# Optimization experiments

Measured on AMD Instinct MI355X. Metric: run time of the kernel, lower is better.

## Reference

```python
import jax, jax.numpy as jnp
import numpy as np

# GPT-2 decoder (mlm=False path of the Keras GPT module), no past/KV-cache,
# no explicit mask -> causal mask, dropout disabled (training=False).
N_HEAD = 12
NINF = -10000.0  # Attention.ninf
EPS = 1e-6


def layer_norm(x, g, b):
    m = jnp.mean(x, axis=-1, keepdims=True)
    v = jnp.mean(jnp.square(x - m), axis=-1, keepdims=True)
    return (x - m) / jnp.sqrt(v + EPS) * g + b


def gelu(x):
    # 0.5*x*(1+erf(x/sqrt(2))) as in gelu_activating
    return 0.5 * x * (1.0 + jax.lax.erf(x * np.float32(1.0 / np.sqrt(2.0))))


def setup_inputs() -> dict:
    key = jax.random.key(0)
    B, S, D, L, V, CTX = 4, 512, 768, 12, 50257, 1024
    F = 4 * D
    ks = jax.random.split(key, 10)
    init = lambda k, shape: (jax.random.normal(k, shape, jnp.float32) * 0.02)
    return {
        "x": jax.random.randint(ks[0], (B, S), 0, V),
        "emb": init(ks[1], (V, D)),        # wte (tied output projection)
        "posemb": init(ks[2], (CTX, D)),   # wpe
        "ln1_g": jnp.ones((L, D)), "ln1_b": jnp.zeros((L, D)),
        "wqkv": init(ks[3], (L, D, 3 * D)), "bqkv": jnp.zeros((L, 3 * D)),
        "wo": init(ks[4], (L, D, D)), "bo": jnp.zeros((L, D)),
        "ln2_g": jnp.ones((L, D)), "ln2_b": jnp.zeros((L, D)),
        "wfc": init(ks[5], (L, D, F)), "bfc": jnp.zeros((L, F)),
        "wproj": init(ks[6], (L, F, D)), "bproj": jnp.zeros((L, D)),
        "lnf_g": jnp.ones((D,)), "lnf_b": jnp.zeros((D,)),
    }


def reference(x, emb, posemb, ln1_g, ln1_b, wqkv, bqkv, wo, bo,
              ln2_g, ln2_b, wfc, bfc, wproj, bproj, lnf_g, lnf_b):
    B, S = x.shape
    L, D, _ = wqkv.shape
    H = N_HEAD
    hd = D // H
    scale = np.float32(1.0 / np.sqrt(hd))

    # Embedding (mlm=False): token + positional, no layernorm
    h = emb[x] + posemb[:S]  # [B,S,D]

    # causal mask: positions j > i get NINF (m1 = range(q)[:,None] < range(k)-k+q)
    mask = (jnp.arange(S)[:, None] < jnp.arange(S)[None, :]).astype(jnp.float32) * NINF

    for i in range(L):
        # pre-norm attention
        qkv = layer_norm(h, ln1_g[i], ln1_b[i]) @ wqkv[i] + bqkv[i]  # [B,S,3D]
        q, k, v = jnp.split(qkv, 3, axis=-1)
        q = q.reshape(B, S, H, hd).transpose(0, 2, 1, 3)  # [B,H,S,hd]
        k = k.reshape(B, S, H, hd).transpose(0, 2, 1, 3)
        v = v.reshape(B, S, H, hd).transpose(0, 2, 1, 3)
        scores = jnp.einsum('bhqd,bhkd->bhqk', q, k) * scale + mask
        a = jax.nn.softmax(scores, axis=-1)  # [B,H,S,S]
        o = jnp.einsum('bhqk,bhkd->bhqd', a, v)
        o = o.transpose(0, 2, 1, 3).reshape(B, S, D)
        h = h + (o @ wo[i] + bo[i])  # residual
        # pre-norm MLP
        m = layer_norm(h, ln2_g[i], ln2_b[i])
        h = h + (gelu(m @ wfc[i] + bfc[i]) @ wproj[i] + bproj[i])

    hidden = layer_norm(h, lnf_g, lnf_b)          # model/lnorm_f
    logits = hidden @ emb.T                        # tied embedding projection
    probs = jax.nn.softmax(logits, axis=-1)        # softmax=True
    return (probs, hidden)
```

## Files before the change

kernel.cpp:

```cpp
#include <hip/hip_runtime.h>
#include <hip/hip_bf16.h>

typedef __bf16 bf16_t;
typedef bf16_t bf16x8 __attribute__((ext_vector_type(8)));
typedef float  f32x4  __attribute__((ext_vector_type(4)));

__device__ __forceinline__ void gload16(const void* g, void* l) {
    __builtin_amdgcn_global_load_lds(
        (const __attribute__((address_space(1))) unsigned int*)g,
        (__attribute__((address_space(3))) unsigned int*)l, 16, 0, 0);
}

__device__ __forceinline__ void drain_and_barrier() {
    __builtin_amdgcn_sched_barrier(0);
    asm volatile("s_waitcnt vmcnt(0)" ::: "memory");
    __builtin_amdgcn_s_barrier();
    __builtin_amdgcn_sched_barrier(0);
}

__global__ void embed_kernel(const int* __restrict__ x,
                             const float* __restrict__ emb,
                             const float* __restrict__ pos,
                             float* __restrict__ h,
                             int S, int D, int total)
{
    int i = blockIdx.x * blockDim.x + threadIdx.x;
    if (i >= total) return;
    int d  = i % D;
    int bs = i / D;
    int s  = bs % S;
    h[i] = emb[(long long)x[bs] * D + d] + pos[(long long)s * D + d];
}

__global__ void convert_bf16(const float* __restrict__ in, bf16_t* __restrict__ out, int n4)
{
    int i = blockIdx.x * blockDim.x + threadIdx.x;
    for (; i < n4; i += gridDim.x * blockDim.x) {
        float4 v = ((const float4*)in)[i];
        bf16_t* o = out + (size_t)i * 4;
        o[0] = (bf16_t)v.x; o[1] = (bf16_t)v.y; o[2] = (bf16_t)v.z; o[3] = (bf16_t)v.w;
    }
}

__global__ __launch_bounds__(256) void transpose_to_bf16(
    const float* __restrict__ in, bf16_t* __restrict__ out, int K, int N)
{
    const float* ip = in  + (size_t)blockIdx.z * K * N;
    bf16_t*      op = out + (size_t)blockIdx.z * K * N;
    __shared__ float t[32][33];
    const int n0 = blockIdx.x * 32, k0 = blockIdx.y * 32;
    const int tx = threadIdx.x, ty = threadIdx.y;
#pragma unroll
    for (int u = 0; u < 4; ++u)
        t[ty + u * 8][tx] = ip[(size_t)(k0 + ty + u * 8) * N + (n0 + tx)];
    __syncthreads();
#pragma unroll
    for (int u = 0; u < 4; ++u)
        op[(size_t)(n0 + ty + u * 8) * K + (k0 + tx)] = (bf16_t)t[tx][ty + u * 8];
}

__global__ __launch_bounds__(256) void layernorm_dual(
    const float* __restrict__ X, const float* __restrict__ g,
    const float* __restrict__ b, bf16_t* __restrict__ Yb,
    float* __restrict__ Yf, int D)
{
    const int row = blockIdx.x;
    const float* xr = X + (long long)row * D;
    const int tid = threadIdx.x;

    float vals[3];
    float s = 0.0f;
#pragma unroll
    for (int u = 0; u < 3; ++u) { vals[u] = xr[tid + u * 256]; s += vals[u]; }

    __shared__ float red[256];
    red[tid] = s;
    __syncthreads();
    for (int off = 128; off > 0; off >>= 1) {
        if (tid < off) red[tid] += red[tid + off];
        __syncthreads();
    }
    const float mean = red[0] / (float)D;
    __syncthreads();

    float vs = 0.0f;
#pragma unroll
    for (int u = 0; u < 3; ++u) { float d = vals[u] - mean; vs += d * d; }
    red[tid] = vs;
    __syncthreads();
    for (int off = 128; off > 0; off >>= 1) {
        if (tid < off) red[tid] += red[tid + off];
        __syncthreads();
    }
    const float var  = red[0] / (float)D;
    const float rstd = rsqrtf(var + 1e-6f);

#pragma unroll
    for (int u = 0; u < 3; ++u) {
        const int c = tid + u * 256;
        const float y = (vals[u] - mean) * rstd * g[c] + b[c];
        Yb[(long long)row * D + c] = (bf16_t)y;
        if (Yf) Yf[(long long)row * D + c] = y;
    }
}

__global__ __launch_bounds__(256) void flash_attn(
    const bf16_t* __restrict__ qkv, bf16_t* __restrict__ o)
{
    constexpr int S = 512, TD = 2304, D = 768, H = 12;
    const int qt = blockIdx.x;
    const int z  = blockIdx.y;
    const int bb = z / H, hh = z - bb * H;
    const int tid = threadIdx.x, lane = tid & 63, w = tid >> 6;
    const int fr = lane & 15, g = lane >> 4, sub = g * 8;

    __shared__ bf16_t kS[2][4096];
    __shared__ bf16_t vS[2][4096];
    __shared__ bf16_t pS[4][16 * 72];

    bf16x8 qf[2];
    const bf16_t* qbase = qkv + (size_t)(bb * S + qt * 64 + w * 16) * TD + hh * 64;
#pragma unroll
    for (int ks = 0; ks < 2; ++ks) {
        bf16x8 v = *(const bf16x8*)&qbase[(size_t)fr * TD + ks * 32 + sub];
#pragma unroll
        for (int j = 0; j < 8; ++j) v[j] = v[j] * (bf16_t)0.125f;
        qf[ks] = v;
    }

    f32x4 oacc[4];
    float mrun[4], lrun[4];
#pragma unroll
    for (int r = 0; r < 4; ++r) { mrun[r] = -3.0e38f; lrun[r] = 0.0f; }
#pragma unroll
    for (int n = 0; n < 4; ++n) oacc[n] = (f32x4){0.f, 0.f, 0.f, 0.f};

    int qr[4];
#pragma unroll
    for (int r = 0; r < 4; ++r) qr[r] = qt * 64 + w * 16 + g * 4 + r;

    const int srow8  = lane >> 3;
    const int schunk = (lane & 7) ^ (srow8 & 7);

    const bf16_t* kGbase = qkv + (size_t)(bb * S) * TD + D + hh * 64;
    const bf16_t* vGbase = qkv + (size_t)(bb * S) * TD + 2 * D + hh * 64;
    const int nkv = qt + 1;

    bf16x8 vreg[2];

#define STAGE_ISSUE(buf, t)                                                     \
    {                                                                           \
        _Pragma("unroll")                                                       \
        for (int it = 0; it < 2; ++it) {                                        \
            const int row = it * 32 + w * 8 + srow8;                            \
            gload16(kGbase + (size_t)((t) * 64 + row) * TD + schunk * 8,        \
                    &kS[buf][it * 2048 + w * 512]);                             \
        }                                                                       \
        _Pragma("unroll")                                                       \
        for (int it = 0; it < 2; ++it) {                                        \
            const int dch = w * 2 + it;                                         \
            vreg[it] = *(const bf16x8*)&vGbase[(size_t)((t) * 64 + lane) * TD + dch * 8]; \
        }                                                                       \
    }
#define STAGE_WRITE(buf)                                                        \
    {                                                                           \
        _Pragma("unroll")                                                       \
        for (int it = 0; it < 2; ++it) {                                        \
            const int dch = w * 2 + it;                                         \
            _Pragma("unroll")                                                   \
            for (int j = 0; j < 8; ++j) {                                       \
                const int d = dch * 8 + j;                                      \
                vS[buf][d * 64 + (((lane >> 3) ^ j) << 3) + (lane & 7)] = vreg[it][j]; \
            }                                                                   \
        }                                                                       \
    }

    STAGE_ISSUE(0, 0);
    STAGE_WRITE(0);
    __syncthreads();

    int cur = 0;
    for (int t = 0; t < nkv; ++t) {
        if (t + 1 < nkv) STAGE_ISSUE(cur ^ 1, t + 1);

        f32x4 sacc[4];
#pragma unroll
        for (int n = 0; n < 4; ++n) sacc[n] = (f32x4){0.f, 0.f, 0.f, 0.f};
#pragma unroll
        for (int ks = 0; ks < 2; ++ks) {
            bf16x8 bK[4];
#pragma unroll
            for (int n = 0; n < 4; ++n) {
                const int rw = n * 16 + fr;
                const int c  = ks * 4 + g;
                bK[n] = *(const bf16x8*)&kS[cur][rw * 64 + ((c ^ (rw & 7)) << 3)];
            }
#pragma unroll
            for (int n = 0; n < 4; ++n)
                sacc[n] = __builtin_amdgcn_mfma_f32_16x16x32_bf16(
                    qf[ks], bK[n], sacc[n], 0, 0, 0);
        }

        if (t == qt) {
#pragma unroll
            for (int n = 0; n < 4; ++n) {
                const int key = t * 64 + n * 16 + fr;
#pragma unroll
                for (int r = 0; r < 4; ++r)
                    if (key > qr[r]) sacc[n][r] = -3.0e38f;
            }
        }

        float sf[4], rs[4];
#pragma unroll
        for (int r = 0; r < 4; ++r) {
            float v = fmaxf(fmaxf(sacc[0][r], sacc[1][r]),
                            fmaxf(sacc[2][r], sacc[3][r]));
#pragma unroll
            for (int off = 1; off < 16; off <<= 1)
                v = fmaxf(v, __shfl_xor(v, off));
            const float mn = fmaxf(mrun[r], v);
            sf[r] = __expf(mrun[r] - mn);
            mrun[r] = mn;
            lrun[r] *= sf[r];
        }
#pragma unroll
        for (int n = 0; n < 4; ++n)
#pragma unroll
            for (int r = 0; r < 4; ++r)
                oacc[n][r] *= sf[r];
#pragma unroll
        for (int r = 0; r < 4; ++r) rs[r] = 0.0f;
#pragma unroll
        for (int n = 0; n < 4; ++n)
#pragma unroll
            for (int r = 0; r < 4; ++r) {
                const float p = __expf(sacc[n][r] - mrun[r]);
                sacc[n][r] = p;
                rs[r] += p;
            }
#pragma unroll
        for (int r = 0; r < 4; ++r) {
            float v = rs[r];
#pragma unroll
            for (int off = 1; off < 16; off <<= 1) v += __shfl_xor(v, off);
            lrun[r] += v;
        }

        bf16_t* pw = pS[w];
#pragma unroll
        for (int n = 0; n < 4; ++n)
#pragma unroll
            for (int r = 0; r < 4; ++r)
                pw[(g * 4 + r) * 72 + n * 16 + fr] = (bf16_t)sacc[n][r];

#pragma unroll
        for (int ks = 0; ks < 2; ++ks) {
            bf16x8 pa, vb[4];
            pa = *(const bf16x8*)&pw[fr * 72 + ks * 32 + sub];
#pragma unroll
            for (int n = 0; n < 4; ++n) {
                const int rw = n * 16 + fr;
                const int c  = ks * 4 + g;
                vb[n] = *(const bf16x8*)&vS[cur][rw * 64 + ((c ^ (rw & 7)) << 3)];
            }
#pragma unroll
            for (int n = 0; n < 4; ++n)
                oacc[n] = __builtin_amdgcn_mfma_f32_16x16x32_bf16(
                    pa, vb[n], oacc[n], 0, 0, 0);
        }

        if (t + 1 < nkv) STAGE_WRITE(cur ^ 1);
        __syncthreads();
        cur ^= 1;
    }
#undef STAGE_ISSUE
#undef STAGE_WRITE

    bf16_t* obase = o + (size_t)(bb * S + qt * 64 + w * 16) * D + hh * 64;
#pragma unroll
    for (int r = 0; r < 4; ++r) {
        const float inv = 1.0f / lrun[r];
#pragma unroll
        for (int n = 0; n < 4; ++n)
            obase[(size_t)(g * 4 + r) * D + n * 16 + fr] =
                (bf16_t)(oacc[n][r] * inv);
    }
}

__global__ __launch_bounds__(256) void softmax_vocab(
    const bf16_t* __restrict__ logits, const float* __restrict__ pmax,
    const float* __restrict__ psum, float* __restrict__ probs,
    int V, int Vp, int NP)
{
    const int tid = threadIdx.x;
    const int row = blockIdx.x;
    const bf16_t* lr = logits + (size_t)row * Vp;
    float* pr = probs + (size_t)row * V;
    const float* pm = pmax + (size_t)row * 400;
    const float* ps = psum + (size_t)row * 400;

    float m = -3.0e38f, s = 0.0f;
    for (int p = tid; p < NP; p += 256) {
        const float om = pm[p], os = ps[p];
        const float M_ = fmaxf(m, om);
        s = s * __expf(m - M_) + os * __expf(om - M_);
        m = M_;
    }

    __shared__ float mS[256], sS[256];
    mS[tid] = m; sS[tid] = s;
    __syncthreads();
    for (int off = 128; off > 0; off >>= 1) {
        if (tid < off) {
            const float m1 = mS[tid], m2 = mS[tid + off];
            const float M_ = fmaxf(m1, m2);
            sS[tid] = sS[tid] * __expf(m1 - M_) + sS[tid + off] * __expf(m2 - M_);
            mS[tid] = M_;
        }
        __syncthreads();
    }
    const float M_  = mS[0];
    const float inv = 1.0f / sS[0];

    const int n8 = V >> 3;
    for (int c8 = tid; c8 < n8; c8 += 256) {
        const bf16x8 v = *(const bf16x8*)(lr + (size_t)c8 * 8);
#pragma unroll
        for (int j = 0; j < 8; ++j)
            pr[(size_t)c8 * 8 + j] = __expf((float)v[j] - M_) * inv;
    }
    for (int c = n8 * 8 + tid; c < V; c += 256)
        pr[c] = __expf((float)lr[c] - M_) * inv;
}

template<bool ADD, bool GELU_, bool OUTBF>
__device__ __forceinline__ void gemm_body(
    const bf16_t* __restrict__ A, const bf16_t* __restrict__ Bw,
    const float* __restrict__ bias, void* __restrict__ Cv,
    int M, int N, int K, int lda, int ldb, int ldc)
{
    constexpr int BUF = 12288;
    __shared__ bf16_t lds[2 * BUF];

    const int tid  = threadIdx.x;
    const int lane = tid & 63;
    const int w    = tid >> 6;
    const int row0 = blockIdx.x * 128;
    const int col0 = blockIdx.y * 64;

    const int row8 = lane >> 3;
    const int sch  = (lane & 7) ^ row8;
    const int fr   = lane & 15;
    const int g    = lane >> 4;

    const int aRowB = row0 + w * 32;
    const int bRowB = col0 + w * 16;

    f32x4 acc[2][4];
#pragma unroll
    for (int m = 0; m < 2; ++m)
#pragma unroll
        for (int n = 0; n < 4; ++n)
            acc[m][n] = (f32x4){0.f, 0.f, 0.f, 0.f};

    auto STAGE = [&](int buf, int k0) {
        bf16_t* lb = lds + buf * BUF;
#pragma unroll
        for (int it = 0; it < 4; ++it) {
            const int ar = aRowB + it * 8 + row8;
            gload16(A + (size_t)ar * lda + k0 + sch * 8, lb + w * 2048 + it * 512);
        }
#pragma unroll
        for (int it = 0; it < 2; ++it) {
            int br = bRowB + it * 8 + row8;
            if (br >= N) br = 0;
            gload16(Bw + (size_t)br * ldb + k0 + sch * 8,
                    lb + 8192 + w * 1024 + it * 512);
        }
    };

    auto COMPUTE = [&](int buf) {
        bf16_t* lb = lds + buf * BUF;
#pragma unroll
        for (int ks = 0; ks < 2; ++ks) {
            bf16x8 af[2], bfr[4];
            const int cs = ks * 4 + g;
#pragma unroll
            for (int m = 0; m < 2; ++m) {
                const int row = w * 32 + m * 16 + fr;
                af[m] = *(const bf16x8*)&lb[row * 64 + ((cs ^ (fr & 7)) << 3)];
            }
#pragma unroll
            for (int n = 0; n < 4; ++n) {
                const int row = n * 16 + fr;
                bfr[n] = *(const bf16x8*)&lb[8192 + row * 64 + ((cs ^ (fr & 7)) << 3)];
            }
#pragma unroll
            for (int m = 0; m < 2; ++m)
#pragma unroll
                for (int n = 0; n < 4; ++n)
                    acc[m][n] = __builtin_amdgcn_mfma_f32_16x16x32_bf16(
                        af[m], bfr[n], acc[m][n], 0, 0, 0);
        }
    };

    const int nt = K >> 6;
    STAGE(0, 0);
    drain_and_barrier();
    int cur = 0;
    for (int t = 0; t < nt; ++t) {
        if (t + 1 < nt) STAGE(cur ^ 1, (t + 1) << 6);
        COMPUTE(cur);
        drain_and_barrier();
        cur ^= 1;
    }

    const int rBase = row0 + w * 32 + g * 4;
    const int cBase = col0 + fr;
    float bv[4];
#pragma unroll
    for (int n = 0; n < 4; ++n) {
        const int c = cBase + n * 16;
        bv[n] = (bias && c < N) ? bias[c] : 0.0f;
    }
#pragma unroll
    for (int m = 0; m < 2; ++m) {
#pragma unroll
        for (int r = 0; r < 4; ++r) {
            const int rr = rBase + m * 16 + r;
#pragma unroll
            for (int n = 0; n < 4; ++n) {
                const int c = cBase + n * 16;
                if (c >= N) continue;
                float v = acc[m][n][r] + bv[n];
                if (GELU_) v = 0.5f * v * (1.0f + erff(v * 0.70710678118654752f));
                if (OUTBF) {
                    ((bf16_t*)Cv)[(size_t)rr * ldc + c] = (bf16_t)v;
                } else {
                    float* Cf = (float*)Cv;
                    const size_t idx = (size_t)rr * ldc + c;
                    if (ADD) v += Cf[idx];
                    Cf[idx] = v;
                }
            }
        }
    }
}

__global__ __launch_bounds__(256) void k_gemm_qkv(
    const bf16_t* A, const bf16_t* B, const float* bias, void* C,
    int M, int N, int K, int lda, int ldb, int ldc)
{ gemm_body<false, false, true>(A, B, bias, C, M, N, K, lda, ldb, ldc); }

__global__ __launch_bounds__(256) void k_gemm_fc(
    const bf16_t* A, const bf16_t* B, const float* bias, void* C,
    int M, int N, int K, int lda, int ldb, int ldc)
{ gemm_body<false, true, true>(A, B, bias, C, M, N, K, lda, ldb, ldc); }

__global__ __launch_bounds__(256) void k_gemm_small(
    const bf16_t* __restrict__ A, const bf16_t* __restrict__ Bw,
    const float* __restrict__ bias, float* __restrict__ C,
    int M, int N, int K, int lda, int ldb, int ldc)
{
    constexpr int BUF = 8192;
    __shared__ bf16_t lds[2 * BUF];

    const int tid  = threadIdx.x;
    const int lane = tid & 63;
    const int w    = tid >> 6;
    const int row0 = blockIdx.x * 64;
    const int col0 = blockIdx.y * 64;

    const int row8 = lane >> 3;
    const int sch  = (lane & 7) ^ row8;
    const int fr   = lane & 15;
    const int g    = lane >> 4;

    f32x4 acc[4];
#pragma unroll
    for (int m = 0; m < 4; ++m) acc[m] = (f32x4){0.f, 0.f, 0.f, 0.f};

    auto STAGE = [&](int buf, int k0) {
        bf16_t* lb = lds + buf * BUF;
#pragma unroll
        for (int it = 0; it < 2; ++it) {
            const int ar = row0 + it * 32 + w * 8 + row8;
            gload16(A + (size_t)ar * lda + k0 + sch * 8,
                    lb + (it * 32 + w * 8) * 64);
            const int br = col0 + it * 32 + w * 8 + row8;
            gload16(Bw + (size_t)br * ldb + k0 + sch * 8,
                    lb + 4096 + (it * 32 + w * 8) * 64);
        }
    };

    auto COMPUTE = [&](int buf) {
        bf16_t* lb = lds + buf * BUF;
#pragma unroll
        for (int ks = 0; ks < 2; ++ks) {
            const int cs = ks * 4 + g;
            const int bRow = w * 16 + fr;
            bf16x8 bfr = *(const bf16x8*)&lb[4096 + bRow * 64 + ((cs ^ (fr & 7)) << 3)];
#pragma unroll
            for (int m = 0; m < 4; ++m) {
                const int row = m * 16 + fr;
                bf16x8 af = *(const bf16x8*)&lb[row * 64 + ((cs ^ (fr & 7)) << 3)];
                acc[m] = __builtin_amdgcn_mfma_f32_16x16x32_bf16(
                    af, bfr, acc[m], 0, 0, 0);
            }
        }
    };

    const int nt = K >> 6;
    STAGE(0, 0);
    drain_and_barrier();
    int cur = 0;
    for (int t = 0; t < nt; ++t) {
        if (t + 1 < nt) STAGE(cur ^ 1, (t + 1) << 6);
        COMPUTE(cur);
        drain_and_barrier();
        cur ^= 1;
    }

    const int c = col0 + w * 16 + fr;
    const float bv = bias ? bias[c] : 0.0f;
#pragma unroll
    for (int m = 0; m < 4; ++m) {
#pragma unroll
        for (int r = 0; r < 4; ++r) {
            const int rr = row0 + m * 16 + g * 4 + r;
            const size_t idx = (size_t)rr * ldc + c;
            C[idx] += acc[m][r] + bv;
        }
    }
}

__global__ __launch_bounds__(256) void k_gemm_head(
    const bf16_t* __restrict__ A, const bf16_t* __restrict__ Bw,
    bf16_t* __restrict__ C, float* __restrict__ pmax, float* __restrict__ psum,
    int M, int N, int K, int lda, int ldb, int ldc)
{
    __shared__ bf16_t lds[16384];

    const int tid  = threadIdx.x;
    const int lane = tid & 63;
    const int w    = tid >> 6;
    const int wr   = w >> 1, wc = w & 1;
    const int row0 = blockIdx.x * 128;
    const int col0 = blockIdx.y * 128;

    const int row8 = lane >> 3;
    const int sch  = (lane & 7) ^ row8;
    const int fr   = lane & 15;
    const int g    = lane >> 4;

    const int aRowB = row0 + w * 32;
    const int bRowB = col0 + w * 32;

    f32x4 acc[4][4];
#pragma unroll
    for (int m = 0; m < 4; ++m)
#pragma unroll
        for (int n = 0; n < 4; ++n)
            acc[m][n] = (f32x4){0.f, 0.f, 0.f, 0.f};

    for (int k0 = 0; k0 < K; k0 += 64) {
#pragma unroll
        for (int it = 0; it < 4; ++it) {
            const int ar = aRowB + it * 8 + row8;
            gload16(A + (size_t)ar * lda + k0 + sch * 8,
                    lds + w * 2048 + it * 512);
            int br = bRowB + it * 8 + row8;
            if (br >= N) br = 0;
            gload16(Bw + (size_t)br * ldb + k0 + sch * 8,
                    lds + 8192 + w * 2048 + it * 512);
        }
        __syncthreads();

#pragma unroll
        for (int ks = 0; ks < 2; ++ks) {
            bf16x8 af[4], bfr[4];
            const int cs = ks * 4 + g;
#pragma unroll
            for (int m = 0; m < 4; ++m) {
                const int row = wr * 64 + m * 16 + fr;
                af[m] = *(const bf16x8*)&lds[row * 64 + ((cs ^ (fr & 7)) << 3)];
            }
#pragma unroll
            for (int n = 0; n < 4; ++n) {
                const int row = wc * 64 + n * 16 + fr;
                bfr[n] = *(const bf16x8*)&lds[8192 + row * 64 + ((cs ^ (fr & 7)) << 3)];
            }
#pragma unroll
            for (int m = 0; m < 4; ++m)
#pragma unroll
                for (int n = 0; n < 4; ++n)
                    acc[m][n] = __builtin_amdgcn_mfma_f32_16x16x32_bf16(
                        af[m], bfr[n], acc[m][n], 0, 0, 0);
        }
        __syncthreads();
    }

    const int rBase = row0 + wr * 64 + g * 4;
    const int cBase = col0 + wc * 64 + fr;
#pragma unroll
    for (int n = 0; n < 4; ++n) {
        const int c = cBase + n * 16;
        if (c >= N) continue;
#pragma unroll
        for (int m = 0; m < 4; ++m)
#pragma unroll
            for (int r = 0; r < 4; ++r)
                C[(size_t)(rBase + m * 16 + r) * ldc + c] = (bf16_t)acc[m][n][r];
    }

    float* sred = (float*)lds;
#pragma unroll
    for (int m = 0; m < 4; ++m) {
#pragma unroll
        for (int r = 0; r < 4; ++r) {
            float lm = -3.0e38f;
#pragma unroll
            for (int n = 0; n < 4; ++n) {
                const int c = cBase + n * 16;
                if (c < N) lm = fmaxf(lm, (float)(bf16_t)acc[m][n][r]);
            }
#pragma unroll
            for (int off = 1; off < 16; off <<= 1)
                lm = fmaxf(lm, __shfl_xor(lm, off));
            float ls = 0.0f;
#pragma unroll
            for (int n = 0; n < 4; ++n) {
                const int c = cBase + n * 16;
                if (c < N) ls += __expf((float)(bf16_t)acc[m][n][r] - lm);
            }
#pragma unroll
            for (int off = 1; off < 16; off <<= 1)
                ls += __shfl_xor(ls, off);
            if (fr == 0) {
                const int rl = wr * 64 + m * 16 + g * 4 + r;
                sred[wc * 128 + rl] = lm;
                sred[256 + wc * 128 + rl] = ls;
            }
        }
    }
    __syncthreads();
    if ((w & 1) == 0) {
        const int rl = (w >> 1) * 64 + lane;
        const float m0 = sred[rl],       m1 = sred[128 + rl];
        const float s0 = sred[256 + rl], s1 = sred[384 + rl];
        const float M_ = fmaxf(m0, m1);
        const float S_ = s0 * __expf(m0 - M_) + s1 * __expf(m1 - M_);
        const size_t grow = row0 + rl;
        pmax[grow * 400 + blockIdx.y] = M_;
        psum[grow * 400 + blockIdx.y] = S_;
    }
}

extern "C" void kernel_launch(void* const* d_in, const int* in_sizes, int n_in,
                              void* d_out, int out_size, void* d_ws, size_t ws_size,
                              hipStream_t stream)
{
    constexpr int B = 4, S = 512, D = 768, L = 12, V = 50257, H = 12, F = 3072;
    constexpr int M  = B * S;
    constexpr int TD = 3 * D;
    constexpr int BH = B * H;
    constexpr int Vp = 50264;
    constexpr int NP = (V + 127) / 128;

    const int*   x    = (const int*)  d_in[0];
    const float* emb  = (const float*)d_in[1];
    const float* pos  = (const float*)d_in[2];
    const float* ln1g = (const float*)d_in[3];
    const float* ln1b = (const float*)d_in[4];
    const float* wqkv = (const float*)d_in[5];
    const float* bqkv = (const float*)d_in[6];
    const float* wo   = (const float*)d_in[7];
    const float* bo   = (const float*)d_in[8];
    const float* ln2g = (const float*)d_in[9];
    const float* ln2b = (const float*)d_in[10];
    const float* wfc  = (const float*)d_in[11];
    const float* bfc  = (const float*)d_in[12];
    const float* wpr  = (const float*)d_in[13];
    const float* bpr  = (const float*)d_in[14];
    const float* lnfg = (const float*)d_in[15];
    const float* lnfb = (const float*)d_in[16];

    float* probs  = (float*)d_out;
    float* hidden = probs + (size_t)M * V;

    char* wsb = (char*)d_ws;
    size_t off = 0;
    auto alloc = [&](size_t bytes) -> char* {
        char* p = wsb + off;
        off += (bytes + 255) & ~(size_t)255;
        return p;
    };
    bf16_t* hid_bf = (bf16_t*)alloc((size_t)M * D * 2);
    bf16_t* embB   = (bf16_t*)alloc((size_t)V * D * 2);
    const size_t trunk_start = off;
    float*  h      = (float*) alloc((size_t)M * D * 4);
    bf16_t* qkv_bf = (bf16_t*)alloc((size_t)M * TD * 2);
    bf16_t* xn_bf  = (bf16_t*)alloc((size_t)M * D * 2);
    bf16_t* o_bf   = (bf16_t*)alloc((size_t)M * D * 2);
    bf16_t* mid_bf = (bf16_t*)alloc((size_t)M * F * 2);
    bf16_t* wqkvT  = (bf16_t*)alloc((size_t)L * D * TD * 2);
    bf16_t* woT    = (bf16_t*)alloc((size_t)L * D * D * 2);
    bf16_t* wfcT   = (bf16_t*)alloc((size_t)L * D * F * 2);
    bf16_t* wprT   = (bf16_t*)alloc((size_t)L * F * D * 2);
    const size_t logits_bytes = (size_t)M * Vp * 2;
    if (off < trunk_start + logits_bytes) off = trunk_start + logits_bytes;
    bf16_t* logits = (bf16_t*)(wsb + trunk_start);
    float* pmax = (float*)alloc((size_t)M * 400 * 4);
    float* psum = (float*)alloc((size_t)M * 400 * 4);

    convert_bf16<<<2048, 256, 0, stream>>>(emb, embB, (V * D) / 4);
    transpose_to_bf16<<<dim3(TD / 32, D / 32, L), dim3(32, 8), 0, stream>>>(wqkv, wqkvT, D, TD);
    transpose_to_bf16<<<dim3(D / 32,  D / 32, L), dim3(32, 8), 0, stream>>>(wo,   woT,   D, D);
    transpose_to_bf16<<<dim3(F / 32,  D / 32, L), dim3(32, 8), 0, stream>>>(wfc,  wfcT,  D, F);
    transpose_to_bf16<<<dim3(D / 32,  F / 32, L), dim3(32, 8), 0, stream>>>(wpr,  wprT,  F, D);

    embed_kernel<<<dim3((M * D + 255) / 256), 256, 0, stream>>>(x, emb, pos, h, S, D, M * D);

    for (int i = 0; i < L; ++i) {
        layernorm_dual<<<M, 256, 0, stream>>>(h, ln1g + (size_t)i * D, ln1b + (size_t)i * D,
                                              xn_bf, nullptr, D);

        k_gemm_qkv<<<dim3(M / 128, TD / 64), 256, 0, stream>>>(
            xn_bf, wqkvT + (size_t)i * D * TD, bqkv + (size_t)i * TD, qkv_bf,
            M, TD, D, D, D, TD);

        flash_attn<<<dim3(S / 64, BH), 256, 0, stream>>>(qkv_bf, o_bf);

        k_gemm_small<<<dim3(M / 64, D / 64), 256, 0, stream>>>(
            o_bf, woT + (size_t)i * D * D, bo + (size_t)i * D, h,
            M, D, D, D, D, D);

        layernorm_dual<<<M, 256, 0, stream>>>(h, ln2g + (size_t)i * D, ln2b + (size_t)i * D,
                                              xn_bf, nullptr, D);

        k_gemm_fc<<<dim3(M / 128, F / 64), 256, 0, stream>>>(
            xn_bf, wfcT + (size_t)i * D * F, bfc + (size_t)i * F, mid_bf,
            M, F, D, D, D, F);

        k_gemm_small<<<dim3(M / 64, D / 64), 256, 0, stream>>>(
            mid_bf, wprT + (size_t)i * F * D, bpr + (size_t)i * D, h,
            M, D, F, F, F, D);
    }

    layernorm_dual<<<M, 256, 0, stream>>>(h, lnfg, lnfb, hid_bf, hidden, D);

    k_gemm_head<<<dim3(M / 128, NP), 256, 0, stream>>>(
        hid_bf, embB, logits, pmax, psum,
        M, V, D, D, D, Vp);

    softmax_vocab<<<M, 256, 0, stream>>>(logits, pmax, psum, probs, V, Vp, NP);
}
```

Baseline: 2.065 ms.

## Move vocab softmax statistics from head GEMM epilogue into softmax kernel

Drops the per-tile row max/sum reduction from the head GEMM epilogue and the pmax/psum buffers. The softmax kernel now makes an extra online-softmax pass over the bf16 logits row to compute max and sum itself. The head GEMM also gains an XCD-aware block index remap to improve L2 locality across chiplets. The cost is an extra read of the 200MB bf16 logits in exchange for a lighter GEMM epilogue.

```diff
diff --git a/kernel.cpp b/kernel.cpp
--- a/kernel.cpp
+++ b/kernel.cpp
@@ -289,23 +289,27 @@
 }
 
 __global__ __launch_bounds__(256) void softmax_vocab(
-    const bf16_t* __restrict__ logits, const float* __restrict__ pmax,
-    const float* __restrict__ psum, float* __restrict__ probs,
-    int V, int Vp, int NP)
+    const bf16_t* __restrict__ logits, float* __restrict__ probs, int V, int Vp)
 {
     const int tid = threadIdx.x;
-    const int row = blockIdx.x;
-    const bf16_t* lr = logits + (size_t)row * Vp;
-    float* pr = probs + (size_t)row * V;
-    const float* pm = pmax + (size_t)row * 400;
-    const float* ps = psum + (size_t)row * 400;
+    const bf16_t* lr = logits + (size_t)blockIdx.x * Vp;
+    float* pr = probs + (size_t)blockIdx.x * V;
+    const int n8 = V >> 3;
 
     float m = -3.0e38f, s = 0.0f;
-    for (int p = tid; p < NP; p += 256) {
-        const float om = pm[p], os = ps[p];
-        const float M_ = fmaxf(m, om);
-        s = s * __expf(m - M_) + os * __expf(om - M_);
-        m = M_;
+    for (int c8 = tid; c8 < n8; c8 += 256) {
+        const bf16x8 v = *(const bf16x8*)(lr + (size_t)c8 * 8);
+        float f[8], lm = -3.0e38f;
+#pragma unroll
+        for (int j = 0; j < 8; ++j) { f[j] = (float)v[j]; lm = fmaxf(lm, f[j]); }
+        if (lm > m) { s *= __expf(m - lm); m = lm; }
+#pragma unroll
+        for (int j = 0; j < 8; ++j) s += __expf(f[j] - m);
+    }
+    for (int c = n8 * 8 + tid; c < V; c += 256) {
+        const float f = (float)lr[c];
+        if (f > m) { s *= __expf(m - f); m = f; }
+        s += __expf(f - m);
     }
 
     __shared__ float mS[256], sS[256];
@@ -323,7 +327,6 @@
     const float M_  = mS[0];
     const float inv = 1.0f / sS[0];
 
-    const int n8 = V >> 3;
     for (int c8 = tid; c8 < n8; c8 += 256) {
         const bf16x8 v = *(const bf16x8*)(lr + (size_t)c8 * 8);
 #pragma unroll
@@ -537,17 +540,25 @@
 
 __global__ __launch_bounds__(256) void k_gemm_head(
     const bf16_t* __restrict__ A, const bf16_t* __restrict__ Bw,
-    bf16_t* __restrict__ C, float* __restrict__ pmax, float* __restrict__ psum,
-    int M, int N, int K, int lda, int ldb, int ldc)
+    bf16_t* __restrict__ C, int M, int N, int K, int lda, int ldb, int ldc)
 {
     __shared__ bf16_t lds[16384];
+
+    const int nwg = gridDim.x * gridDim.y;
+    int flat = blockIdx.y * gridDim.x + blockIdx.x;
+    {
+        const int xcd = flat & 7, pos = flat >> 3;
+        flat = xcd * (nwg >> 3) + pos;
+    }
+    const int bx = flat % gridDim.x;
+    const int by = flat / gridDim.x;
 
     const int tid  = threadIdx.x;
     const int lane = tid & 63;
     const int w    = tid >> 6;
     const int wr   = w >> 1, wc = w & 1;
-    const int row0 = blockIdx.x * 128;
-    const int col0 = blockIdx.y * 128;
+    const int row0 = bx * 128;
+    const int col0 = by * 128;
 
     const int row8 = lane >> 3;
     const int sch  = (lane & 7) ^ row8;
@@ -612,48 +623,6 @@
 #pragma unroll
             for (int r = 0; r < 4; ++r)
                 C[(size_t)(rBase + m * 16 + r) * ldc + c] = (bf16_t)acc[m][n][r];
-    }
-
-    float* sred = (float*)lds;
-#pragma unroll
-    for (int m = 0; m < 4; ++m) {
-#pragma unroll
-        for (int r = 0; r < 4; ++r) {
-            float lm = -3.0e38f;
-#pragma unroll
-            for (int n = 0; n < 4; ++n) {
-                const int c = cBase + n * 16;
-                if (c < N) lm = fmaxf(lm, (float)(bf16_t)acc[m][n][r]);
-            }
-#pragma unroll
-            for (int off = 1; off < 16; off <<= 1)
-                lm = fmaxf(lm, __shfl_xor(lm, off));
-            float ls = 0.0f;
-#pragma unroll
-            for (int n = 0; n < 4; ++n) {
-                const int c = cBase + n * 16;
-                if (c < N) ls += __expf((float)(bf16_t)acc[m][n][r] - lm);
-            }
-#pragma unroll
-            for (int off = 1; off < 16; off <<= 1)
-                ls += __shfl_xor(ls, off);
-            if (fr == 0) {
-                const int rl = wr * 64 + m * 16 + g * 4 + r;
-                sred[wc * 128 + rl] = lm;
-                sred[256 + wc * 128 + rl] = ls;
-            }
-        }
-    }
-    __syncthreads();
-    if ((w & 1) == 0) {
-        const int rl = (w >> 1) * 64 + lane;
-        const float m0 = sred[rl],       m1 = sred[128 + rl];
-        const float s0 = sred[256 + rl], s1 = sred[384 + rl];
-        const float M_ = fmaxf(m0, m1);
-        const float S_ = s0 * __expf(m0 - M_) + s1 * __expf(m1 - M_);
-        const size_t grow = row0 + rl;
-        pmax[grow * 400 + blockIdx.y] = M_;
-        psum[grow * 400 + blockIdx.y] = S_;
     }
 }
 
@@ -711,8 +680,6 @@
     const size_t logits_bytes = (size_t)M * Vp * 2;
     if (off < trunk_start + logits_bytes) off = trunk_start + logits_bytes;
     bf16_t* logits = (bf16_t*)(wsb + trunk_start);
-    float* pmax = (float*)alloc((size_t)M * 400 * 4);
-    float* psum = (float*)alloc((size_t)M * 400 * 4);
 
     convert_bf16<<<2048, 256, 0, stream>>>(emb, embB, (V * D) / 4);
     transpose_to_bf16<<<dim3(TD / 32, D / 32, L), dim3(32, 8), 0, stream>>>(wqkv, wqkvT, D, TD);
@@ -751,8 +718,8 @@
     layernorm_dual<<<M, 256, 0, stream>>>(h, lnfg, lnfb, hid_bf, hidden, D);
 
     k_gemm_head<<<dim3(M / 128, NP), 256, 0, stream>>>(
-        hid_bf, embB, logits, pmax, psum,
+        hid_bf, embB, logits,
         M, V, D, D, D, Vp);
 
-    softmax_vocab<<<M, 256, 0, stream>>>(logits, pmax, psum, probs, V, Vp, NP);
-}
+    softmax_vocab<<<M, 256, 0, stream>>>(logits, probs, V, Vp);
+}
```

Result: no change. 2.034 ms (-1.5%).
